# Kernel tuning notes

Hardware: AMD Instinct MI355X
Metric: run time of the kernel (lower is better)

## Reference

```python
import jax, jax.numpy as jnp
import numpy as np

N0, N1, N2 = 400000, 75000, 15000
E1, E2 = 1200000, 240000
F_IN, NC = 64, 40
H1, C1 = 2, 8          # layer 1: heads=2, out_channels=8 -> concat dim 16
H2, C2 = 1, NC         # layer 2: heads=1, out_channels=num_classes
NEG_SLOPE = 0.2


def gat_conv(x_src, x_dst, src, dst, Ws, Wd, att_s, att_d, bias, heads, ch):
    """PyG GATConv on bipartite (x_src, x_dst) with remove+add self loops."""
    n_dst = x_dst.shape[0]
    hs = (x_src @ Ws).reshape(-1, heads, ch)   # [N_src, H, C]
    hd = (x_dst @ Wd).reshape(-1, heads, ch)   # [N_dst, H, C]
    a_s = (hs * att_s).sum(-1)                 # [N_src, H]
    a_d = (hd * att_d).sum(-1)                 # [N_dst, H]
    loops = jnp.arange(n_dst)
    src_all = jnp.concatenate([src, loops])
    dst_all = jnp.concatenate([dst, loops])
    # remove_self_loops: drop pre-existing i->i edges; add_self_loops: appended
    valid = jnp.concatenate([src != dst, jnp.ones(n_dst, dtype=bool)])[:, None]
    logits = jax.nn.leaky_relu(a_s[src_all] + a_d[dst_all], NEG_SLOPE)  # [E, H]
    logits = jnp.where(valid, logits, -jnp.inf)
    m = jax.ops.segment_max(logits, dst_all, num_segments=n_dst)        # [N_dst, H]
    w = jnp.where(valid, jnp.exp(logits - m[dst_all]), 0.0)
    denom = jax.ops.segment_sum(w, dst_all, num_segments=n_dst)
    alpha = w / denom[dst_all]                                          # [E, H]
    out = jax.ops.segment_sum(alpha[:, :, None] * hs[src_all], dst_all,
                              num_segments=n_dst)                       # [N_dst, H, C]
    return out.reshape(n_dst, heads * ch) + bias


def setup_inputs() -> dict:
    key = jax.random.key(0)
    ks = jax.random.split(key, 16)
    s = 0.1
    return {
        "x": jax.random.normal(ks[0], (N0, F_IN), dtype=jnp.float32),
        "e1_src": jax.random.randint(ks[1], (E1,), 0, N0),
        "e1_dst": jax.random.randint(ks[2], (E1,), 0, N1),
        "e2_src": jax.random.randint(ks[3], (E2,), 0, N1),
        "e2_dst": jax.random.randint(ks[4], (E2,), 0, N2),
        "W1s": jax.random.normal(ks[5], (F_IN, H1 * C1), dtype=jnp.float32) * s,
        "W1d": jax.random.normal(ks[6], (F_IN, H1 * C1), dtype=jnp.float32) * s,
        "att1_s": jax.random.normal(ks[7], (H1, C1), dtype=jnp.float32) * s,
        "att1_d": jax.random.normal(ks[8], (H1, C1), dtype=jnp.float32) * s,
        "b1": jnp.zeros((H1 * C1,), dtype=jnp.float32),
        "W2s": jax.random.normal(ks[9], (H1 * C1, H2 * C2), dtype=jnp.float32) * s,
        "W2d": jax.random.normal(ks[10], (H1 * C1, H2 * C2), dtype=jnp.float32) * s,
        "att2_s": jax.random.normal(ks[11], (H2, C2), dtype=jnp.float32) * s,
        "att2_d": jax.random.normal(ks[12], (H2, C2), dtype=jnp.float32) * s,
        "b2": jnp.zeros((H2 * C2,), dtype=jnp.float32),
    }


def reference(x, e1_src, e1_dst, e2_src, e2_dst,
              W1s, W1d, att1_s, att1_d, b1,
              W2s, W2d, att2_s, att2_d, b2):
    h = gat_conv(x, x[:N1], e1_src, e1_dst, W1s, W1d, att1_s, att1_d, b1, H1, C1)
    h = jax.nn.elu(h)
    o = gat_conv(h, h[:N2], e2_src, e2_dst, W2s, W2d, att2_s, att2_d, b2, H2, C2)
    return jax.nn.log_softmax(o, axis=-1)
```

## Files before the change

### kernel.cpp

```cpp
#include <hip/hip_runtime.h>
#include <hip/hip_bf16.h>

constexpr int N0 = 400000, N1 = 75000, N2 = 15000;
constexpr int E1 = 1200000, E2 = 240000;
constexpr int NC = 40;
constexpr float NEG_SLOPE = 0.2f;

constexpr int BK1 = 128;
constexpr int NB1 = (N1 + BK1 - 1) / BK1;
constexpr int CAPB1 = 2432;
constexpr int BK2 = 32;
constexpr int NB2 = (N2 + BK2 - 1) / BK2;
constexpr int CAPB2 = 704;

constexpr int TILE = 4096;
constexpr int NT1L = (E1 + TILE - 1) / TILE;
constexpr int NT2L = (E2 + TILE - 1) / TILE;
constexpr int NTB = NT1L + NT2L;
constexpr int SUBCAP = 32;
constexpr int BPJ = N0 / 64;

using f32x4 = __attribute__((ext_vector_type(4))) float;
using s16x8 = __attribute__((ext_vector_type(8))) short;

__device__ __forceinline__ float leaky(float v) { return v > 0.f ? v : NEG_SLOPE * v; }

__device__ __forceinline__ unsigned cvtpk(float lo, float hi) {
    unsigned r;
    asm("v_cvt_pk_bf16_f32 %0, %1, %2" : "=v"(r) : "v"(lo), "v"(hi));
    return r;
}

__device__ __forceinline__ unsigned bf16pair(float lo, float hi) {
    unsigned a = __float_as_uint(lo), b = __float_as_uint(hi);
    a = (a + 0x7FFFu + ((a >> 16) & 1u)) >> 16;
    b = (b + 0x7FFFu + ((b >> 16) & 1u)) & 0xFFFF0000u;
    return a | b;
}
__device__ __forceinline__ float bfLo(unsigned w) { return __uint_as_float(w << 16); }
__device__ __forceinline__ float bfHi(unsigned w) { return __uint_as_float(w & 0xFFFF0000u); }

__global__ __launch_bounds__(256) void k1_kernel(
    const float* __restrict__ x,
    const float* __restrict__ W1s, const float* __restrict__ W1d,
    const float* __restrict__ att1s, const float* __restrict__ att1d,
    const int* __restrict__ e1s, const int* __restrict__ e1d,
    const int* __restrict__ e2s, const int* __restrict__ e2d,
    unsigned* __restrict__ rec1, float* __restrict__ a_d1,
    int* __restrict__ gcnt1, unsigned* __restrict__ bin1,
    int* __restrict__ gcnt2, unsigned* __restrict__ bin2)
{
    __shared__ int cur[NB1];
    __shared__ float2 vds[64];

    int bid = blockIdx.x;
    const int tid = threadIdx.x;
    if (bid < NTB) {
        const bool isL1 = bid < NT1L;
        const int t = isL1 ? bid : bid - NT1L;
        const int* es = isL1 ? e1s : e2s;
        const int* ed = isL1 ? e1d : e2d;
        const int nE = isL1 ? E1 : E2;
        const int nb = isL1 ? NB1 : NB2;
        const int shift = isL1 ? 7 : 5;
        const int lsh = isL1 ? 19 : 17;
        int* gc = isL1 ? gcnt1 : gcnt2;
        unsigned* gbin = isL1 ? bin1 : bin2;
        const int base = t * TILE;
        const int lim = min(TILE, nE - base);

        for (int b = tid; b < nb; b += 256) cur[b] = 0;
        __syncthreads();
        for (int i = tid; i < lim; i += 256) {
            int s = es[base + i], d = ed[base + i];
            if (s != d) {
                int b = d >> shift;
                int pos = atomicAdd(&cur[b], 1);
                if (pos < SUBCAP)
                    gbin[((size_t)t * nb + b) * SUBCAP + pos] =
                        (unsigned)s | ((unsigned)(d & ((1 << shift) - 1)) << lsh);
            }
        }
        __syncthreads();
        for (int b = tid; b < nb; b += 256)
            gc[(size_t)t * nb + b] = min(cur[b], SUBCAP);
        return;
    }
    bid -= NTB;
    const int l  = tid & 63;
    const int nd = l & 15;
    const int kg = l >> 4;
    const int wv = tid >> 6;
    const int nodeBase = bid * 64;
    const bool hasN1 = nodeBase < N1;

    if (hasN1) {
        if (tid < 64) {
            float d0 = 0.f, d1 = 0.f;
            const float* wr = W1d + (size_t)tid * 16;
            #pragma unroll
            for (int cc = 0; cc < 8; ++cc) {
                d0 = fmaf(wr[cc], att1d[cc], d0);
                d1 = fmaf(wr[8 + cc], att1d[8 + cc], d1);
            }
            vds[tid] = make_float2(d0, d1);
        }
        __syncthreads();
    }

    const int node = nodeBase + wv * 16 + nd;

    const float* xr_ = x + (size_t)node * 64 + 8 * kg;
    float4 q0 = *(const float4*)(xr_);
    float4 q1 = *(const float4*)(xr_ + 4);
    float4 q2 = *(const float4*)(xr_ + 32);
    float4 q3 = *(const float4*)(xr_ + 36);

    s16x8 bf0, bf1;
    {
        union { unsigned u[4]; s16x8 v; } t0, t1;
        #pragma unroll
        for (int q = 0; q < 4; ++q) {
            t0.u[q] = cvtpk(W1s[(8 * kg + 2 * q) * 16 + nd],
                            W1s[(8 * kg + 2 * q + 1) * 16 + nd]);
            t1.u[q] = cvtpk(W1s[(32 + 8 * kg + 2 * q) * 16 + nd],
                            W1s[(32 + 8 * kg + 2 * q + 1) * 16 + nd]);
        }
        bf0 = t0.v; bf1 = t1.v;
    }
    float att4[4];
    #pragma unroll
    for (int r = 0; r < 4; ++r) att4[r] = att1s[4 * kg + r];

    union { unsigned u[4]; s16x8 v; } a0, a1;
    a0.u[0] = cvtpk(q0.x, q0.y); a0.u[1] = cvtpk(q0.z, q0.w);
    a0.u[2] = cvtpk(q1.x, q1.y); a0.u[3] = cvtpk(q1.z, q1.w);
    a1.u[0] = cvtpk(q2.x, q2.y); a1.u[1] = cvtpk(q2.z, q2.w);
    a1.u[2] = cvtpk(q3.x, q3.y); a1.u[3] = cvtpk(q3.z, q3.w);

    f32x4 acc = {0.f, 0.f, 0.f, 0.f};
    acc = __builtin_amdgcn_mfma_f32_16x16x32_bf16(bf0, a0.v, acc, 0, 0, 0);
    acc = __builtin_amdgcn_mfma_f32_16x16x32_bf16(bf1, a1.v, acc, 0, 0, 0);

    float p = acc[0] * att4[0];
    p = fmaf(acc[1], att4[1], p);
    p = fmaf(acc[2], att4[2], p);
    p = fmaf(acc[3], att4[3], p);
    p += __shfl_xor(p, 16, 64);
    float q = __shfl_xor(p, 32, 64);

    unsigned* rp = rec1 + (size_t)node * 16;
    uint2 hw;
    hw.x = cvtpk(acc[0], acc[1]);
    hw.y = cvtpk(acc[2], acc[3]);
    *(uint2*)(rp + 2 * kg) = hw;
    if (kg == 0)
        *(uint4*)(rp + 8) = make_uint4(__float_as_uint(p), __float_as_uint(q), 0u, 0u);
    else if (kg == 1)
        *(uint4*)(rp + 12) = make_uint4(0u, 0u, 0u, 0u);

    if (hasN1 && node < N1) {
        float xv8[16] = {q0.x, q0.y, q0.z, q0.w, q1.x, q1.y, q1.z, q1.w,
                         q2.x, q2.y, q2.z, q2.w, q3.x, q3.y, q3.z, q3.w};
        float pd0 = 0.f, pd1 = 0.f;
        #pragma unroll
        for (int j = 0; j < 8; ++j) {
            float2 v = vds[8 * kg + j];
            pd0 = fmaf(xv8[j], v.x, pd0);
            pd1 = fmaf(xv8[j], v.y, pd1);
        }
        #pragma unroll
        for (int j = 0; j < 8; ++j) {
            float2 v = vds[32 + 8 * kg + j];
            pd0 = fmaf(xv8[8 + j], v.x, pd0);
            pd1 = fmaf(xv8[8 + j], v.y, pd1);
        }
        pd0 += __shfl_xor(pd0, 16, 64); pd0 += __shfl_xor(pd0, 32, 64);
        pd1 += __shfl_xor(pd1, 16, 64); pd1 += __shfl_xor(pd1, 32, 64);
        if (kg == 0)
            ((float2*)a_d1)[node] = make_float2(pd0, pd1);
    }
}

__global__ __launch_bounds__(512) void k2_kernel(
    const int* __restrict__ gcnt1, const unsigned* __restrict__ bin1,
    const unsigned* __restrict__ rec1, const float* __restrict__ a_d1,
    const float* __restrict__ b1,
    const float* __restrict__ W2s, const float* __restrict__ W2d,
    const float* __restrict__ att2s, const float* __restrict__ att2d,
    unsigned* __restrict__ rec2)
{
    __shared__ unsigned raw[CAPB1];
    __shared__ unsigned srt[CAPB1];
    __shared__ int cnts[NT1L], pfx[NT1L + 1];
    __shared__ int hist[BK1], start[BK1 + 1];
    __shared__ float w2sl[640], va[16], vd[16];
    __shared__ float h1s[BK1][17];

    const int b = blockIdx.x, tid = threadIdx.x;
    const int d0 = b * BK1;
    const int nN = min(BK1, N1 - d0);

    for (int i = tid; i < 640; i += 512) w2sl[i] = W2s[i];
    if (tid < BK1) hist[tid] = 0;
    if (tid >= 128 && tid < 144) {
        int k = tid - 128;
        float sa = 0.f, sd = 0.f;
        for (int cc = 0; cc < 40; ++cc) {
            sa = fmaf(W2s[k * 40 + cc], att2s[cc], sa);
            sd = fmaf(W2d[k * 40 + cc], att2d[cc], sd);
        }
        va[k] = sa; vd[k] = sd;
    }
    for (int i = tid; i < NT1L; i += 512) cnts[i] = gcnt1[(size_t)i * NB1 + b];
    __syncthreads();
    if (tid < 64) {
        int carry = 0;
        #pragma unroll
        for (int s = 0; s < (NT1L + 63) / 64; ++s) {
            int idx = s * 64 + tid;
            int v = (idx < NT1L) ? cnts[idx] : 0;
            int xv = v;
            #pragma unroll
            for (int d = 1; d < 64; d <<= 1) {
                int t2 = __shfl_up(xv, d, 64);
                if (tid >= d) xv += t2;
            }
            if (idx < NT1L) pfx[idx] = carry + xv - v;
            carry += __shfl(xv, 63, 64);
        }
        if (tid == 0) pfx[NT1L] = carry;
    }
    __syncthreads();
    for (int j = tid; j < NT1L * SUBCAP; j += 512) {
        int t = j >> 5, p = j & (SUBCAP - 1);
        if (p < cnts[t]) {
            int dst = pfx[t] + p;
            if (dst < CAPB1) {
                unsigned pay = bin1[((size_t)t * NB1 + b) * SUBCAP + p];
                raw[dst] = pay;
                atomicAdd(&hist[pay >> 19], 1);
            }
        }
    }
    __syncthreads();
    if (tid == 0) {
        int a = 0;
        for (int k = 0; k < BK1; ++k) { start[k] = a; a += hist[k]; }
        start[BK1] = a;
    }
    __syncthreads();
    if (tid < BK1) hist[tid] = start[tid];
    __syncthreads();
    const int total = min(pfx[NT1L], CAPB1);
    for (int i = tid; i < total; i += 512) {
        unsigned p = raw[i];
        int pos = atomicAdd(&hist[p >> 19], 1);
        srt[pos] = p & 0x7FFFFu;
    }
    __syncthreads();

    const int g = tid >> 4, c = tid & 15, h = c >> 3;
    const int wbase = tid & 48;
    const int wmap = (c < 8) ? c : (8 + ((c >> 2) & 1));
    for (int n = g; n < nN; n += 32) {
        const int node = d0 + n;
        const float ad = a_d1[(size_t)node * 2 + h];
        const int st = start[n], cnt = start[n + 1] - start[n];
        unsigned rw0 = rec1[(size_t)node * 16 + wmap];
        unsigned rw1 = (cnt >= 1) ? rec1[(size_t)srt[st] * 16 + wmap] : 0u;
        unsigned rw2 = (cnt >= 2) ? rec1[(size_t)srt[st + 1] * 16 + wmap] : 0u;
        unsigned rw3 = (cnt >= 3) ? rec1[(size_t)srt[st + 2] * 16 + wmap] : 0u;
        float accv = 0.f, den = 0.f;
        for (int j = 0; j <= cnt; ++j) {
            float asv = __uint_as_float((unsigned)__shfl((int)rw0, wbase + 8 + 4 * h, 64));
            unsigned chw = (unsigned)__shfl((int)rw0, wbase + (c >> 1), 64);
            float hv = (c & 1) ? bfHi(chw) : bfLo(chw);
            float w = __expf(leaky(asv + ad));
            accv = fmaf(w, hv, accv);
            den += w;
            rw0 = rw1; rw1 = rw2; rw2 = rw3;
            rw3 = (j + 4 <= cnt) ? rec1[(size_t)srt[st + j + 3] * 16 + wmap] : 0u;
        }
        float v = accv / den + b1[c];
        h1s[n][c] = v > 0.f ? v : (__expf(v) - 1.f);
    }
    __syncthreads();
    for (int i = tid; i < nN * 24; i += 512) {
        int nn = i / 24, w = i - nn * 24;
        unsigned* rp = rec2 + (size_t)(d0 + nn) * 24;
        if (w < 20) {
            int c0 = 2 * w, c1 = c0 + 1;
            float s0 = 0.f, s1 = 0.f;
            #pragma unroll
            for (int k = 0; k < 16; ++k) {
                float hk = h1s[nn][k];
                s0 = fmaf(hk, w2sl[k * 40 + c0], s0);
                s1 = fmaf(hk, w2sl[k * 40 + c1], s1);
            }
            rp[w] = bf16pair(s0, s1);
        } else if (w < 22) {
            const float* vv = (w == 20) ? va : vd;
            float s = 0.f;
            #pragma unroll
            for (int k = 0; k < 16; ++k) s = fmaf(h1s[nn][k], vv[k], s);
            rp[w] = __float_as_uint(s);
        }
    }
}

__global__ __launch_bounds__(1024) void k3_kernel(
    const int* __restrict__ gcnt2, const unsigned* __restrict__ bin2,
    const unsigned* __restrict__ rec2, const float* __restrict__ b2,
    float* __restrict__ out)
{
    __shared__ unsigned raw[CAPB2];
    __shared__ unsigned srt[CAPB2];
    __shared__ int cnts[NT2L], pfx[NT2L + 1];
    __shared__ int hist[BK2], start[BK2 + 1];

    const int b = blockIdx.x, tid = threadIdx.x;
    const int d0 = b * BK2;
    const int nN = min(BK2, N2 - d0);

    if (tid < BK2) hist[tid] = 0;
    if (tid < NT2L) cnts[tid] = gcnt2[(size_t)tid * NB2 + b];
    __syncthreads();
    if (tid < 64) {
        int v = (tid < NT2L) ? cnts[tid] : 0;
        int xv = v;
        #pragma unroll
        for (int d = 1; d < 64; d <<= 1) {
            int t2 = __shfl_up(xv, d, 64);
            if (tid >= d) xv += t2;
        }
        if (tid < NT2L) pfx[tid] = xv - v;
        if (tid == NT2L - 1) pfx[NT2L] = xv;
    }
    __syncthreads();
    for (int j = tid; j < NT2L * SUBCAP; j += 1024) {
        int t = j >> 5, p = j & (SUBCAP - 1);
        if (p < cnts[t]) {
            int dst = pfx[t] + p;
            if (dst < CAPB2) {
                unsigned pay = bin2[((size_t)t * NB2 + b) * SUBCAP + p];
                raw[dst] = pay;
                atomicAdd(&hist[pay >> 17], 1);
            }
        }
    }
    __syncthreads();
    if (tid == 0) {
        int a = 0;
        for (int k = 0; k < BK2; ++k) { start[k] = a; a += hist[k]; }
        start[BK2] = a;
    }
    __syncthreads();
    if (tid < BK2) hist[tid] = start[tid];
    __syncthreads();
    const int total = min(pfx[NT2L], CAPB2);
    for (int i = tid; i < total; i += 1024) {
        unsigned p = raw[i];
        int pos = atomicAdd(&hist[p >> 17], 1);
        srt[pos] = p & 0x1FFFFu;
    }
    __syncthreads();

    const int g = tid >> 5, l = tid & 31;
    const float bb0 = (l < 20) ? b2[2 * l] : 0.f;
    const float bb1 = (l < 20) ? b2[2 * l + 1] : 0.f;
    for (int n = g; n < nN; n += 32) {
        const int node = d0 + n;
        const int st = start[n], cnt = start[n + 1] - start[n];
        unsigned rw0 = (l < 22) ? rec2[(size_t)node * 24 + l] : 0u;
        const float ad = __uint_as_float((unsigned)__shfl((int)rw0, 21, 32));
        unsigned rw1 = (cnt >= 1 && l < 21) ? rec2[(size_t)srt[st] * 24 + l] : 0u;
        unsigned rw2 = (cnt >= 2 && l < 21) ? rec2[(size_t)srt[st + 1] * 24 + l] : 0u;
        unsigned rw3 = (cnt >= 3 && l < 21) ? rec2[(size_t)srt[st + 2] * 24 + l] : 0u;
        float a0 = 0.f, a1 = 0.f, den = 0.f;
        for (int j = 0; j <= cnt; ++j) {
            float asv = __uint_as_float((unsigned)__shfl((int)rw0, 20, 32));
            float w = __expf(leaky(asv + ad));
            a0 = fmaf(w, bfLo(rw0), a0);
            a1 = fmaf(w, bfHi(rw0), a1);
            den += w;
            rw0 = rw1; rw1 = rw2; rw2 = rw3;
            rw3 = (j + 4 <= cnt && l < 21) ? rec2[(size_t)srt[st + j + 3] * 24 + l] : 0u;
        }
        float v0 = (l < 20) ? a0 / den + bb0 : -3.4e38f;
        float v1 = (l < 20) ? a1 / den + bb1 : -3.4e38f;
        float mx = fmaxf(v0, v1);
        #pragma unroll
        for (int k = 16; k >= 1; k >>= 1) mx = fmaxf(mx, __shfl_xor(mx, k, 32));
        float ex = (l < 20) ? __expf(v0 - mx) + __expf(v1 - mx) : 0.f;
        #pragma unroll
        for (int k = 16; k >= 1; k >>= 1) ex += __shfl_xor(ex, k, 32);
        float lse = mx + logf(ex);
        if (l < 20)
            ((float2*)(out + (size_t)node * 40))[l] = make_float2(v0 - lse, v1 - lse);
    }
}

extern "C" void kernel_launch(void* const* d_in, const int* in_sizes, int n_in,
                              void* d_out, int out_size, void* d_ws, size_t ws_size,
                              hipStream_t stream) {
    const float* x      = (const float*)d_in[0];
    const int*   e1_src = (const int*)d_in[1];
    const int*   e1_dst = (const int*)d_in[2];
    const int*   e2_src = (const int*)d_in[3];
    const int*   e2_dst = (const int*)d_in[4];
    const float* W1s    = (const float*)d_in[5];
    const float* W1d    = (const float*)d_in[6];
    const float* att1s  = (const float*)d_in[7];
    const float* att1d  = (const float*)d_in[8];
    const float* b1     = (const float*)d_in[9];
    const float* W2s    = (const float*)d_in[10];
    const float* W2d    = (const float*)d_in[11];
    const float* att2s  = (const float*)d_in[12];
    const float* att2d  = (const float*)d_in[13];
    const float* b2     = (const float*)d_in[14];
    float* out = (float*)d_out;

    float* wsbase = (float*)d_ws;
    size_t o = 0;
    int*      gcnt1 = (int*)(wsbase + o);      o += (size_t)NT1L * NB1;
    int*      gcnt2 = (int*)(wsbase + o);      o += (size_t)NT2L * NB2;
    unsigned* bin1  = (unsigned*)(wsbase + o); o += (size_t)NT1L * NB1 * SUBCAP;
    unsigned* bin2  = (unsigned*)(wsbase + o); o += (size_t)NT2L * NB2 * SUBCAP;
    unsigned* rec1  = (unsigned*)(wsbase + o); o += (size_t)N0 * 16;
    float*    a_d1  = (float*)(wsbase + o);    o += (size_t)N1 * 2;
    unsigned* rec2  = (unsigned*)(wsbase + o); o += (size_t)N1 * 24;

    k1_kernel<<<NTB + BPJ, 256, 0, stream>>>(
        x, W1s, W1d, att1s, att1d, e1_src, e1_dst, e2_src, e2_dst,
        rec1, a_d1, gcnt1, bin1, gcnt2, bin2);

    k2_kernel<<<NB1, 512, 0, stream>>>(gcnt1, bin1, rec1, a_d1, b1,
                                       W2s, W2d, att2s, att2d, rec2);

    k3_kernel<<<NB2, 1024, 0, stream>>>(gcnt2, bin2, rec2, b2, out);
}
```

Baseline: 115.8 us.

## Coalesce x loads via LDS staging and interleave two destination nodes in aggregation

The projection part of k1 now has each block cover 256 nodes, looping four 16-node tiles per wave. Each tile's x rows are loaded contiguously with coalesced float4 reads and transposed through a padded LDS stage, replacing per-lane strided row loads. Separately, the layer-1 aggregation in k2 processes two destination nodes per group at once with interleaved prefetch chains, aiming to hide gather latency through extra memory-level parallelism. The cost is more registers, wasted iterations when the two nodes' degrees differ, and the k2 loop now assumes at most 128 nodes per bucket.

After: 112.6 us. 2.7% less time.

```diff
diff --git a/kernel.cpp b/kernel.cpp
--- a/kernel.cpp
+++ b/kernel.cpp
@@ -18,7 +18,7 @@
 constexpr int NT2L = (E2 + TILE - 1) / TILE;
 constexpr int NTB = NT1L + NT2L;
 constexpr int SUBCAP = 32;
-constexpr int BPJ = N0 / 64;
+constexpr int BPJ = (N0 + 255) / 256;
 
 using f32x4 = __attribute__((ext_vector_type(4))) float;
 using s16x8 = __attribute__((ext_vector_type(8))) short;
@@ -50,8 +50,9 @@
     int* __restrict__ gcnt1, unsigned* __restrict__ bin1,
     int* __restrict__ gcnt2, unsigned* __restrict__ bin2)
 {
-    __shared__ int cur[NB1];
+    __shared__ float4 stage[4][272];
     __shared__ float2 vds[64];
+    int* cur = (int*)stage;
 
     int bid = blockIdx.x;
     const int tid = threadIdx.x;
@@ -91,7 +92,7 @@
     const int nd = l & 15;
     const int kg = l >> 4;
     const int wv = tid >> 6;
-    const int nodeBase = bid * 64;
+    const int nodeBase = bid * 256;
     const bool hasN1 = nodeBase < N1;
 
     if (hasN1) {
@@ -107,14 +108,6 @@
         }
         __syncthreads();
     }
-
-    const int node = nodeBase + wv * 16 + nd;
-
-    const float* xr_ = x + (size_t)node * 64 + 8 * kg;
-    float4 q0 = *(const float4*)(xr_);
-    float4 q1 = *(const float4*)(xr_ + 4);
-    float4 q2 = *(const float4*)(xr_ + 32);
-    float4 q3 = *(const float4*)(xr_ + 36);
 
     s16x8 bf0, bf1;
     {
@@ -132,53 +125,80 @@
     #pragma unroll
     for (int r = 0; r < 4; ++r) att4[r] = att1s[4 * kg + r];
 
-    union { unsigned u[4]; s16x8 v; } a0, a1;
-    a0.u[0] = cvtpk(q0.x, q0.y); a0.u[1] = cvtpk(q0.z, q0.w);
-    a0.u[2] = cvtpk(q1.x, q1.y); a0.u[3] = cvtpk(q1.z, q1.w);
-    a1.u[0] = cvtpk(q2.x, q2.y); a1.u[1] = cvtpk(q2.z, q2.w);
-    a1.u[2] = cvtpk(q3.x, q3.y); a1.u[3] = cvtpk(q3.z, q3.w);
-
-    f32x4 acc = {0.f, 0.f, 0.f, 0.f};
-    acc = __builtin_amdgcn_mfma_f32_16x16x32_bf16(bf0, a0.v, acc, 0, 0, 0);
-    acc = __builtin_amdgcn_mfma_f32_16x16x32_bf16(bf1, a1.v, acc, 0, 0, 0);
-
-    float p = acc[0] * att4[0];
-    p = fmaf(acc[1], att4[1], p);
-    p = fmaf(acc[2], att4[2], p);
-    p = fmaf(acc[3], att4[3], p);
-    p += __shfl_xor(p, 16, 64);
-    float q = __shfl_xor(p, 32, 64);
-
-    unsigned* rp = rec1 + (size_t)node * 16;
-    uint2 hw;
-    hw.x = cvtpk(acc[0], acc[1]);
-    hw.y = cvtpk(acc[2], acc[3]);
-    *(uint2*)(rp + 2 * kg) = hw;
-    if (kg == 0)
-        *(uint4*)(rp + 8) = make_uint4(__float_as_uint(p), __float_as_uint(q), 0u, 0u);
-    else if (kg == 1)
-        *(uint4*)(rp + 12) = make_uint4(0u, 0u, 0u, 0u);
-
-    if (hasN1 && node < N1) {
-        float xv8[16] = {q0.x, q0.y, q0.z, q0.w, q1.x, q1.y, q1.z, q1.w,
-                         q2.x, q2.y, q2.z, q2.w, q3.x, q3.y, q3.z, q3.w};
-        float pd0 = 0.f, pd1 = 0.f;
-        #pragma unroll
-        for (int j = 0; j < 8; ++j) {
-            float2 v = vds[8 * kg + j];
-            pd0 = fmaf(xv8[j], v.x, pd0);
-            pd1 = fmaf(xv8[j], v.y, pd1);
-        }
-        #pragma unroll
-        for (int j = 0; j < 8; ++j) {
-            float2 v = vds[32 + 8 * kg + j];
-            pd0 = fmaf(xv8[8 + j], v.x, pd0);
-            pd1 = fmaf(xv8[8 + j], v.y, pd1);
-        }
-        pd0 += __shfl_xor(pd0, 16, 64); pd0 += __shfl_xor(pd0, 32, 64);
-        pd1 += __shfl_xor(pd1, 16, 64); pd1 += __shfl_xor(pd1, 32, 64);
+    float4* st = stage[wv];
+    const int wslot = (l >> 4);
+    const int wlane = (l & 15);
+
+    #pragma unroll
+    for (int t = 0; t < 4; ++t) {
+        const int tile0 = nodeBase + wv * 64 + t * 16;
+        if (tile0 >= N0) break;
+
+        const float4* xg = (const float4*)x + (size_t)tile0 * 16;
+        float4 v0 = xg[0 * 64 + l];
+        float4 v1 = xg[1 * 64 + l];
+        float4 v2 = xg[2 * 64 + l];
+        float4 v3 = xg[3 * 64 + l];
+
+        st[(0 * 4 + wslot) * 17 + wlane] = v0;
+        st[(1 * 4 + wslot) * 17 + wlane] = v1;
+        st[(2 * 4 + wslot) * 17 + wlane] = v2;
+        st[(3 * 4 + wslot) * 17 + wlane] = v3;
+        float4 p0 = st[nd * 17 + 2 * kg];
+        float4 p1 = st[nd * 17 + 2 * kg + 1];
+        float4 p2 = st[nd * 17 + 8 + 2 * kg];
+        float4 p3 = st[nd * 17 + 8 + 2 * kg + 1];
+
+        const int node = tile0 + nd;
+
+        union { unsigned u[4]; s16x8 v; } a0, a1;
+        a0.u[0] = cvtpk(p0.x, p0.y); a0.u[1] = cvtpk(p0.z, p0.w);
+        a0.u[2] = cvtpk(p1.x, p1.y); a0.u[3] = cvtpk(p1.z, p1.w);
+        a1.u[0] = cvtpk(p2.x, p2.y); a1.u[1] = cvtpk(p2.z, p2.w);
+        a1.u[2] = cvtpk(p3.x, p3.y); a1.u[3] = cvtpk(p3.z, p3.w);
+
+        f32x4 acc = {0.f, 0.f, 0.f, 0.f};
+        acc = __builtin_amdgcn_mfma_f32_16x16x32_bf16(bf0, a0.v, acc, 0, 0, 0);
+        acc = __builtin_amdgcn_mfma_f32_16x16x32_bf16(bf1, a1.v, acc, 0, 0, 0);
+
+        float p = acc[0] * att4[0];
+        p = fmaf(acc[1], att4[1], p);
+        p = fmaf(acc[2], att4[2], p);
+        p = fmaf(acc[3], att4[3], p);
+        p += __shfl_xor(p, 16, 64);
+        float q = __shfl_xor(p, 32, 64);
+
+        unsigned* rp = rec1 + (size_t)node * 16;
+        uint2 hw;
+        hw.x = cvtpk(acc[0], acc[1]);
+        hw.y = cvtpk(acc[2], acc[3]);
+        *(uint2*)(rp + 2 * kg) = hw;
         if (kg == 0)
-            ((float2*)a_d1)[node] = make_float2(pd0, pd1);
+            *(uint4*)(rp + 8) = make_uint4(__float_as_uint(p), __float_as_uint(q), 0u, 0u);
+        else if (kg == 1)
+            *(uint4*)(rp + 12) = make_uint4(0u, 0u, 0u, 0u);
+
+        if (hasN1 && node < N1) {
+            float xv8[16] = {p0.x, p0.y, p0.z, p0.w, p1.x, p1.y, p1.z, p1.w,
+                             p2.x, p2.y, p2.z, p2.w, p3.x, p3.y, p3.z, p3.w};
+            float pd0 = 0.f, pd1 = 0.f;
+            #pragma unroll
+            for (int j = 0; j < 8; ++j) {
+                float2 v = vds[8 * kg + j];
+                pd0 = fmaf(xv8[j], v.x, pd0);
+                pd1 = fmaf(xv8[j], v.y, pd1);
+            }
+            #pragma unroll
+            for (int j = 0; j < 8; ++j) {
+                float2 v = vds[32 + 8 * kg + j];
+                pd0 = fmaf(xv8[8 + j], v.x, pd0);
+                pd1 = fmaf(xv8[8 + j], v.y, pd1);
+            }
+            pd0 += __shfl_xor(pd0, 16, 64); pd0 += __shfl_xor(pd0, 32, 64);
+            pd1 += __shfl_xor(pd1, 16, 64); pd1 += __shfl_xor(pd1, 32, 64);
+            if (kg == 0)
+                ((float2*)a_d1)[node] = make_float2(pd0, pd1);
+        }
     }
 }
 
@@ -263,27 +283,55 @@
     const int g = tid >> 4, c = tid & 15, h = c >> 3;
     const int wbase = tid & 48;
     const int wmap = (c < 8) ? c : (8 + ((c >> 2) & 1));
-    for (int n = g; n < nN; n += 32) {
-        const int node = d0 + n;
-        const float ad = a_d1[(size_t)node * 2 + h];
-        const int st = start[n], cnt = start[n + 1] - start[n];
-        unsigned rw0 = rec1[(size_t)node * 16 + wmap];
-        unsigned rw1 = (cnt >= 1) ? rec1[(size_t)srt[st] * 16 + wmap] : 0u;
-        unsigned rw2 = (cnt >= 2) ? rec1[(size_t)srt[st + 1] * 16 + wmap] : 0u;
-        unsigned rw3 = (cnt >= 3) ? rec1[(size_t)srt[st + 2] * 16 + wmap] : 0u;
-        float accv = 0.f, den = 0.f;
-        for (int j = 0; j <= cnt; ++j) {
-            float asv = __uint_as_float((unsigned)__shfl((int)rw0, wbase + 8 + 4 * h, 64));
-            unsigned chw = (unsigned)__shfl((int)rw0, wbase + (c >> 1), 64);
-            float hv = (c & 1) ? bfHi(chw) : bfLo(chw);
-            float w = __expf(leaky(asv + ad));
-            accv = fmaf(w, hv, accv);
-            den += w;
-            rw0 = rw1; rw1 = rw2; rw2 = rw3;
-            rw3 = (j + 4 <= cnt) ? rec1[(size_t)srt[st + j + 3] * 16 + wmap] : 0u;
-        }
-        float v = accv / den + b1[c];
-        h1s[n][c] = v > 0.f ? v : (__expf(v) - 1.f);
+    for (int n0 = g; n0 < 64; n0 += 32) {
+        const int nA = n0, nB = n0 + 64;
+        const bool vB = nB < nN;
+        const int nodeA = d0 + nA, nodeB = d0 + min(nB, nN - 1);
+        const float adA = a_d1[(size_t)nodeA * 2 + h];
+        const float adB = a_d1[(size_t)nodeB * 2 + h];
+        const int stA = start[nA], cntA = start[nA + 1] - stA;
+        const int stB = vB ? start[nB] : 0;
+        const int cntB = vB ? (start[nB + 1] - stB) : -1;
+
+        unsigned rwA0 = rec1[(size_t)nodeA * 16 + wmap];
+        unsigned rwA1 = (cntA >= 1) ? rec1[(size_t)srt[stA] * 16 + wmap] : 0u;
+        unsigned rwA2 = (cntA >= 2) ? rec1[(size_t)srt[stA + 1] * 16 + wmap] : 0u;
+        unsigned rwB0 = vB ? rec1[(size_t)nodeB * 16 + wmap] : 0u;
+        unsigned rwB1 = (cntB >= 1) ? rec1[(size_t)srt[stB] * 16 + wmap] : 0u;
+        unsigned rwB2 = (cntB >= 2) ? rec1[(size_t)srt[stB + 1] * 16 + wmap] : 0u;
+
+        float accA = 0.f, denA = 0.f, accB = 0.f, denB = 0.f;
+        const int mx = max(cntA, cntB);
+        for (int j = 0; j <= mx; ++j) {
+            {
+                float asv = __uint_as_float((unsigned)__shfl((int)rwA0, wbase + 8 + 4 * h, 64));
+                unsigned chw = (unsigned)__shfl((int)rwA0, wbase + (c >> 1), 64);
+                float hv = (c & 1) ? bfHi(chw) : bfLo(chw);
+                float w = (j <= cntA) ? __expf(leaky(asv + adA)) : 0.f;
+                accA = fmaf(w, hv, accA);
+                denA += w;
+            }
+            {
+                float asv = __uint_as_float((unsigned)__shfl((int)rwB0, wbase + 8 + 4 * h, 64));
+                unsigned chw = (unsigned)__shfl((int)rwB0, wbase + (c >> 1), 64);
+                float hv = (c & 1) ? bfHi(chw) : bfLo(chw);
+                float w = (j <= cntB) ? __expf(leaky(asv + adB)) : 0.f;
+                accB = fmaf(w, hv, accB);
+                denB += w;
+            }
+            rwA0 = rwA1; rwA1 = rwA2;
+            rwA2 = (j + 3 <= cntA) ? rec1[(size_t)srt[stA + j + 2] * 16 + wmap] : 0u;
+            rwB0 = rwB1; rwB1 = rwB2;
+            rwB2 = (j + 3 <= cntB) ? rec1[(size_t)srt[stB + j + 2] * 16 + wmap] : 0u;
+        }
+        {
+            float v = accA / denA + b1[c];
+            h1s[nA][c] = v > 0.f ? v : (__expf(v) - 1.f);
+        }
+        if (vB) {
+            float v = accB / denB + b1[c];
+            h1s[nB][c] = v > 0.f ? v : (__expf(v) - 1.f);
+        }
     }
     __syncthreads();
     for (int i = tid; i < nN * 24; i += 512) {
```
